# Kernel tuning notes

Hardware: AMD Instinct MI355X
Metric: run time of the kernel (lower is better)

The kernel has to match this reference:

```python
import jax, jax.numpy as jnp
import numpy as np

EM_DIM = 64
GROUP = 16
DIM_IN = 1024


def _position_embedding(boxes, part_boxes):
    # boxes: [N,4], part_boxes: [P,4] -> [N,P,EM_DIM]
    xmin, ymin, xmax, ymax = [boxes[:, i:i + 1] for i in range(4)]            # [N,1]
    pxmin, pymin, pxmax, pymax = [part_boxes[:, i:i + 1].T for i in range(4)]  # [1,P]
    bw = xmax - xmin + 1.0
    bh = ymax - ymin + 1.0
    pw = pxmax - pxmin + 1.0
    ph = pymax - pymin + 1.0
    cx = 0.5 * (xmin + xmax)
    cy = 0.5 * (ymin + ymax)
    pcx = 0.5 * (pxmin + pxmax)
    pcy = 0.5 * (pymin + pymax)
    dx = jnp.abs((cx - pcx) / bw)
    dy = jnp.abs((cy - pcy) / bh)
    dx = jnp.log(jnp.where(dx < 1e-3, 1e-3, dx))
    dy = jnp.log(jnp.where(dy < 1e-3, 1e-3, dy))
    dw = jnp.log(pw / bw)
    dh = jnp.log(ph / bh)
    pos = jnp.stack([dx, dy, dw, dh], axis=2)                                  # [N,P,4]
    em_range = jnp.arange(EM_DIM // 8, dtype=pos.dtype) / (EM_DIM // 8)        # [8]
    em_mat = jnp.power(jnp.asarray(1000.0, pos.dtype), em_range)               # [8]
    div = (100.0 * pos)[..., None] / em_mat                                    # [N,P,4,8]
    emb = jnp.concatenate([jnp.sin(div), jnp.cos(div)], axis=3)                # [N,P,4,16]
    return emb.reshape(pos.shape[0], pos.shape[1], EM_DIM)


def _single_relation(boxes, part_boxes, bf, pf, Wg_w, Wg_b, Wq_w, Wq_b, Wk_w, Wk_b, conv_w, conv_b):
    N = bf.shape[0]
    P = pf.shape[0]
    emb = _position_embedding(boxes, part_boxes)                               # [N,P,64]
    pos_feat = jax.nn.relu(emb @ Wg_w.T + Wg_b)                                # [N,P,G]
    att_weight = jnp.transpose(pos_feat, (0, 2, 1))                            # [N,G,P]
    q = (bf @ Wq_w.T + Wq_b).reshape(N, GROUP, EM_DIM)                         # [N,G,64]
    k = (pf @ Wk_w.T + Wk_b).reshape(P, GROUP, EM_DIM)                         # [P,G,64]
    att = jnp.einsum('ngd,pgd->ngp', q, k) * (1.0 / GROUP)                     # [N,G,P]
    att_weight = jnp.where(att_weight < 1e-6, 1e-6, att_weight)
    sm = jax.nn.softmax(jnp.log(att_weight) + att, axis=2)                     # [N,G,P]
    out = jnp.einsum('ngp,pc->ngc', sm, pf)                                    # [N,G,dim_in]
    # grouped 1x1 conv: group g maps dim_in channels -> EM_DIM channels
    w3 = conv_w.reshape(GROUP, EM_DIM, DIM_IN)
    rel = jnp.einsum('ngc,goc->ngo', out, w3).reshape(N, GROUP * EM_DIM) + conv_b
    return rel                                                                  # [N, G*EM_DIM]


def setup_inputs() -> dict:
    key = jax.random.key(0)
    ks = jax.random.split(key, 12)
    N_TOT, P_TOT = 2048, 2048

    def make_rois(k1, k2, n, n1):
        xy = jax.random.uniform(k1, (n, 2), jnp.float32) * 800.0
        wh = jax.random.uniform(k2, (n, 2), jnp.float32) * 200.0 + 16.0
        boxes = jnp.concatenate([xy, xy + wh], axis=1)
        idx = jnp.concatenate([jnp.zeros((n1, 1)), jnp.ones((n - n1, 1))], axis=0).astype(jnp.float32)
        return jnp.concatenate([idx, boxes], axis=1)

    rois = make_rois(ks[0], ks[1], N_TOT, 1024)
    part_rois = make_rois(ks[2], ks[3], P_TOT, 1024)
    box_feats = jax.random.normal(ks[4], (N_TOT, DIM_IN), jnp.float32)
    part_feats = jax.random.normal(ks[5], (P_TOT, DIM_IN), jnp.float32)
    xav_g = float(np.sqrt(6.0 / (EM_DIM + GROUP)))
    xav_qk = float(np.sqrt(6.0 / (DIM_IN + GROUP * EM_DIM)))
    Wg_w = jax.random.uniform(ks[6], (GROUP, EM_DIM), jnp.float32, -xav_g, xav_g)
    Wg_b = jnp.zeros((GROUP,), jnp.float32)
    Wq_w = jax.random.uniform(ks[7], (GROUP * EM_DIM, DIM_IN), jnp.float32, -xav_qk, xav_qk)
    Wq_b = jnp.zeros((GROUP * EM_DIM,), jnp.float32)
    Wk_w = jax.random.uniform(ks[8], (GROUP * EM_DIM, DIM_IN), jnp.float32, -xav_qk, xav_qk)
    Wk_b = jnp.zeros((GROUP * EM_DIM,), jnp.float32)
    conv_w = jax.random.normal(ks[9], (GROUP * EM_DIM, DIM_IN), jnp.float32) * 0.02
    conv_b = jnp.zeros((GROUP * EM_DIM,), jnp.float32)
    return {"rois": rois, "part_rois": part_rois, "box_feats": box_feats,
            "part_feats": part_feats, "Wg_w": Wg_w, "Wg_b": Wg_b,
            "Wq_w": Wq_w, "Wq_b": Wq_b, "Wk_w": Wk_w, "Wk_b": Wk_b,
            "conv_w": conv_w, "conv_b": conv_b, "n1_boxes": 1024, "n1_parts": 1024}


def reference(rois, part_rois, box_feats, part_feats, Wg_w, Wg_b, Wq_w, Wq_b,
              Wk_w, Wk_b, conv_w, conv_b, n1_boxes, n1_parts):
    boxes = rois[:, 1:5]
    part_boxes = part_rois[:, 1:5]
    params = (Wg_w, Wg_b, Wq_w, Wq_b, Wk_w, Wk_b, conv_w, conv_b)
    rel1 = _single_relation(boxes[:n1_boxes], part_boxes[:n1_parts],
                            box_feats[:n1_boxes], part_feats[:n1_parts], *params)
    rel2 = _single_relation(boxes[n1_boxes:], part_boxes[n1_parts:],
                            box_feats[n1_boxes:], part_feats[n1_parts:], *params)
    return jnp.concatenate([rel1, rel2], axis=0)  # [N_total, GROUP*EM_DIM]
```

## Files before the change

### kernel.cpp

```cpp
#include <hip/hip_runtime.h>

typedef unsigned short u16;
using short8  = __attribute__((ext_vector_type(8))) short;
using float4v = __attribute__((ext_vector_type(4))) float;

__device__ __forceinline__ u16 f2bf(float f) {
    union { float f; unsigned u; } v; v.f = f;
    unsigned r = (v.u + 0x7fff + ((v.u >> 16) & 1)) >> 16;
    return (u16)r;
}
__device__ __forceinline__ float bf2f(u16 h) {
    union { unsigned u; float f; } v; v.u = ((unsigned)h) << 16; return v.f;
}
__device__ __forceinline__ unsigned pkbf(float lo, float hi) {
    unsigned d;
    asm("v_cvt_pk_bf16_f32 %0, %1, %2" : "=v"(d) : "v"(lo), "v"(hi));
    return d;
}
__device__ __forceinline__ float sin_rev(float r) {
    float f, s;
    asm("v_fract_f32 %0, %1" : "=v"(f) : "v"(r));
    asm("v_sin_f32 %0, %1" : "=v"(s) : "v"(f));
    return s;
}
__device__ __forceinline__ void dma16(const void* g, void* l) {
    __builtin_amdgcn_global_load_lds((const __attribute__((address_space(1))) void*)g,
                                     (__attribute__((address_space(3))) void*)l, 16, 0, 0);
}

__device__ __forceinline__ void cvt4(const float* __restrict__ s, u16* __restrict__ o, int i) {
    float4 v = ((const float4*)s)[i];
    uint2 r; r.x = pkbf(v.x, v.y); r.y = pkbf(v.z, v.w);
    ((uint2*)o)[i] = r;
}

__global__ __launch_bounds__(256)
void cvt_all(const float* __restrict__ s0, const float* __restrict__ s1,
             const float* __restrict__ s2, const float* __restrict__ s3,
             const float* __restrict__ s4, const float* __restrict__ prois,
             u16* __restrict__ o0, u16* __restrict__ o1, u16* __restrict__ o2,
             u16* __restrict__ o3, u16* __restrict__ o4, float4* __restrict__ PD,
             int na4, int nb4, int nw4, int PT) {
    int i = blockIdx.x * 256 + threadIdx.x;
    if (i < na4) { cvt4(s0, o0, i); return; }
    i -= na4;
    if (i < nb4) { cvt4(s1, o1, i); return; }
    i -= nb4;
    if (i < nw4) { cvt4(s2, o2, i); return; }
    i -= nw4;
    if (i < nw4) { cvt4(s3, o3, i); return; }
    i -= nw4;
    if (i < nw4) { cvt4(s4, o4, i); return; }
    i -= nw4;
    if (i < PT) {
        const float* pr = prois + (size_t)i * 5;
        float pxmin = pr[1], pymin = pr[2], pxmax = pr[3], pymax = pr[4];
        PD[i] = make_float4(0.5f * (pxmin + pxmax), 0.5f * (pymin + pymax),
                            __logf(pxmax - pxmin + 1.0f), __logf(pymax - pymin + 1.0f));
    }
}

__global__ __launch_bounds__(256)
void proj_posw(const u16* __restrict__ Ab, const u16* __restrict__ Pb,
               const u16* __restrict__ Wqb, const u16* __restrict__ Wkb,
               const u16* __restrict__ Cwb, const float* __restrict__ bq,
               const float* __restrict__ bk, u16* __restrict__ Qb,
               u16* __restrict__ Kb, u16* __restrict__ PVt,
               const float* __restrict__ rois, const float4* __restrict__ PD,
               const float* __restrict__ Wg_w, const float* __restrict__ Wg_b,
               u16* __restrict__ POSW, const int* __restrict__ n1b_p,
               const int* __restrict__ n1p_p, int PT) {
    __shared__ __align__(16) u16 SH[16896];

    const int grp = blockIdx.x / 11, rem = blockIdx.x % 11;
    const int t = threadIdx.x;
    const int w = t >> 6, lane = t & 63;
    const int fm = lane & 15, quad = lane >> 4;

    if (rem < 3) {
        u16* As = SH;
        u16* Ws = SH + 8192;
        u16* Tr = SH;
        const int pb = grp * 3 + rem;
        const int z = pb >> 8;
        const int m0 = ((pb >> 4) & 15) * 128, j0 = (pb & 15) * 64;
        const u16* A = (z == 0) ? Ab : Pb;
        const u16* W = (z == 0) ? Wqb : (z == 1 ? Wkb : Cwb);
        const int wm = w >> 1, wn = w & 1;
        const int lr = lane >> 3, lc = lane & 7, gch = lc ^ lr;

        float4v zero4 = {0.f, 0.f, 0.f, 0.f};
        float4v acc[4][2];
#pragma unroll
        for (int i = 0; i < 4; ++i) { acc[i][0] = zero4; acc[i][1] = zero4; }

        for (int k0 = 0; k0 < 1024; k0 += 64) {
#pragma unroll
            for (int i = 0; i < 4; ++i) {
                int row = w * 32 + i * 8 + lr;
                dma16(A + (size_t)(m0 + row) * 1024 + k0 + gch * 8,
                      As + (w * 32 + i * 8) * 64 + lane * 8);
            }
#pragma unroll
            for (int i = 0; i < 2; ++i) {
                int row = w * 16 + i * 8 + lr;
                dma16(W + (size_t)(j0 + row) * 1024 + k0 + gch * 8,
                      Ws + (w * 16 + i * 8) * 64 + lane * 8);
            }
            __syncthreads();
#pragma unroll
            for (int ks = 0; ks < 2; ++ks) {
                int c = ks * 4 + quad;
                short8 af[4], bf[2];
#pragma unroll
                for (int i = 0; i < 4; ++i) {
                    int ra = wm * 64 + i * 16 + fm;
                    af[i] = *(const short8*)(As + ra * 64 + ((c ^ (ra & 7)) * 8));
                }
#pragma unroll
                for (int j = 0; j < 2; ++j) {
                    int rb = wn * 32 + j * 16 + fm;
                    bf[j] = *(const short8*)(Ws + rb * 64 + ((c ^ (rb & 7)) * 8));
                }
#pragma unroll
                for (int i = 0; i < 4; ++i)
#pragma unroll
                    for (int j = 0; j < 2; ++j)
                        acc[i][j] = __builtin_amdgcn_mfma_f32_16x16x32_bf16(af[i], bf[j], acc[i][j], 0, 0, 0);
            }
            __syncthreads();
        }

        if (z < 2) {
            u16* O = z ? Kb : Qb;
            const float* bias = z ? bk : bq;
#pragma unroll
            for (int j = 0; j < 2; ++j) {
                int jl = wn * 32 + j * 16 + fm;
                float bb = bias[j0 + jl];
#pragma unroll
                for (int i = 0; i < 4; ++i) {
                    int mlb = wm * 64 + i * 16 + quad * 4;
#pragma unroll
                    for (int r = 0; r < 4; ++r)
                        Tr[(mlb + r) * 68 + jl] = f2bf(acc[i][j][r] + bb);
                }
            }
            __syncthreads();
#pragma unroll
            for (int i2 = 0; i2 < 4; ++i2) {
                int f = i2 * 2048 + t * 8;
                int ml = f >> 6, jl = f & 63;
                union { uint2 u2[2]; short8 s8; } uu;
                uu.u2[0] = *(const uint2*)(Tr + ml * 68 + jl);
                uu.u2[1] = *(const uint2*)(Tr + ml * 68 + jl + 4);
                *(short8*)(O + (size_t)(m0 + ml) * 1024 + j0 + jl) = uu.s8;
            }
        } else {
#pragma unroll
            for (int j = 0; j < 2; ++j) {
                int jl = wn * 32 + j * 16 + fm;
#pragma unroll
                for (int i = 0; i < 4; ++i) {
                    int mlb = wm * 64 + i * 16 + quad * 4;
                    uint2 pk;
                    pk.x = pkbf(acc[i][j][0], acc[i][j][1]);
                    pk.y = pkbf(acc[i][j][2], acc[i][j][3]);
                    *(uint2*)(Tr + jl * 136 + mlb) = pk;
                }
            }
            __syncthreads();
#pragma unroll
            for (int i2 = 0; i2 < 4; ++i2) {
                int f = i2 * 2048 + t * 8;
                int jl = f >> 7, ml = f & 127;
                union { uint2 u2[2]; short8 s8; } uu;
                uu.u2[0] = *(const uint2*)(Tr + jl * 136 + ml);
                uu.u2[1] = *(const uint2*)(Tr + jl * 136 + ml + 4);
                *(short8*)(PVt + (size_t)(j0 + jl) * PT + m0 + ml) = uu.s8;
            }
        }
        return;
    }

    u16* Wl = SH + w * 4224;

    const int n = grp * 8 + (rem - 3);
    const int n1b = *n1b_p, n1p = *n1p_p;
    const int hh = (n >= n1b) ? 1 : 0;
    const int p0 = hh ? n1p : 0;
    const int Ph = hh ? (PT - n1p) : n1p;

    float xmin = rois[n * 5 + 1], ymin = rois[n * 5 + 2];
    float xmax = rois[n * 5 + 3], ymax = rois[n * 5 + 4];
    float bw = xmax - xmin + 1.0f, bh = ymax - ymin + 1.0f;
    float cx = 0.5f * (xmin + xmax), cy = 0.5f * (ymin + ymax);

    const int jA = quad >> 1, trig = quad & 1;
    float cA   = (jA == 0) ? cx : cy;
    float invA = (jA == 0) ? (1.0f / bw) : (1.0f / bh);
    float lB   = (jA == 0) ? __logf(bw) : __logf(bh);
    float toff = trig ? 0.25f : 0.0f;

    const int g_ = fm;
    short8 b1, b2;
    {
        const float* w1 = Wg_w + g_ * 64 + quad * 8;
        const float* w2 = Wg_w + g_ * 64 + 32 + quad * 8;
        unsigned* p1 = (unsigned*)&b1;
        unsigned* p2 = (unsigned*)&b2;
#pragma unroll
        for (int kk = 0; kk < 4; ++kk) {
            p1[kk] = pkbf(w1[2 * kk], w1[2 * kk + 1]);
            p2[kk] = pkbf(w2[2 * kk], w2[2 * kk + 1]);
        }
    }
    float wgb = Wg_b[g_];

    const float inv_em[8] = {1.0f, 0.4216965034f, 0.1778279410f, 0.0749894209f,
                             0.0316227766f, 0.0133352143f, 0.0056234133f, 0.0023713737f};
    const float REV = 15.91549431f;
    const int prange = Ph >> 2;
    const int pb0 = w * prange;

    float4 pd_c = PD[p0 + pb0 + fm];

#pragma unroll 2
    for (int pt = 0; pt < 16; ++pt) {
        float4 pd_n;
        if (pt < 15) pd_n = PD[p0 + pb0 + pt * 16 + 16 + fm];
        float pc = (jA == 0) ? pd_c.x : pd_c.y;
        float lp = (jA == 0) ? pd_c.z : pd_c.w;
        float posA = __logf(fmaxf(fabsf(cA - pc) * invA, 0.001f));
        float posB = lp - lB;
        float br1 = posA * REV, br2 = posB * REV;
        float e1[8], e2[8];
#pragma unroll
        for (int k = 0; k < 8; ++k) {
            e1[k] = sin_rev(fmaf(br1, inv_em[k], toff));
            e2[k] = sin_rev(fmaf(br2, inv_em[k], toff));
        }
        short8 a1, a2;
        unsigned* pa1 = (unsigned*)&a1;
        unsigned* pa2 = (unsigned*)&a2;
#pragma unroll
        for (int kk = 0; kk < 4; ++kk) {
            pa1[kk] = pkbf(e1[2 * kk], e1[2 * kk + 1]);
            pa2[kk] = pkbf(e2[2 * kk], e2[2 * kk + 1]);
        }
        float4v acc = {wgb, wgb, wgb, wgb};
        acc = __builtin_amdgcn_mfma_f32_16x16x32_bf16(a1, b1, acc, 0, 0, 0);
        acc = __builtin_amdgcn_mfma_f32_16x16x32_bf16(a2, b2, acc, 0, 0, 0);

        float w0  = fmaxf(acc[0], 1e-6f);
        float w1v = fmaxf(acc[1], 1e-6f);
        float w2v = fmaxf(acc[2], 1e-6f);
        float w3v = fmaxf(acc[3], 1e-6f);
        uint2 wp; wp.x = pkbf(w0, w1v); wp.y = pkbf(w2v, w3v);
        *(uint2*)(Wl + pt * 264 + lane * 4) = wp;

        pd_c = pd_n;
    }

    const int p8 = (lane & 31) * 8;
    const int halfg = lane >> 5;
    const int itq = p8 >> 4;
    const int q0 = (p8 >> 2) & 3;
#pragma unroll
    for (int s = 0; s < 8; ++s) {
        int gg = s * 2 + halfg;
        union { uint2 u2[2]; short8 s8; } uu;
        uu.u2[0] = *(const uint2*)(Wl + itq * 264 + (q0 * 16 + gg) * 4);
        uu.u2[1] = *(const uint2*)(Wl + itq * 264 + ((q0 + 1) * 16 + gg) * 4);
        *(short8*)(POSW + ((size_t)n * 16 + gg) * 1024 + pb0 + p8) = uu.s8;
    }
}

__global__ __launch_bounds__(256)
void fused_rel(const u16* __restrict__ Qb, const u16* __restrict__ Kb,
               const u16* __restrict__ POSW, const u16* __restrict__ PVt,
               const float* __restrict__ conv_b, float* __restrict__ OUT,
               const int* __restrict__ n1b_p, const int* __restrict__ n1p_p, int PT) {
    __shared__ __align__(16) u16 Qs[64 * 64];
    __shared__ __align__(16) u16 Ks[2][64 * 64];
    __shared__ __align__(16) u16 Ps[2][64 * 64];
    __shared__ __align__(16) u16 Vs[2][64 * 64];
    __shared__ __align__(16) u16 Wt[4][16 * 64];

    const int n0 = blockIdx.x * 64, g = blockIdx.y;
    const int n1b = *n1b_p, n1p = *n1p_p;
    const int hh = (n0 >= n1b) ? 1 : 0;
    const int p0 = hh ? n1p : 0;
    const int Ph = hh ? (PT - n1p) : n1p;
    const int t = threadIdx.x;
    const int w = t >> 6, lane = t & 63;
    const int lr = lane >> 3, lc = lane & 7, gch = lc ^ lr;
    const int fm = lane & 15, quad = lane >> 4;
    const int swz = fm & 7;

    const int row0 = w * 16 + lr, row1 = w * 16 + 8 + lr;
    const size_t kb0 = (size_t)(p0 + row0) * 1024 + g * 64 + gch * 8;
    const size_t kb1 = (size_t)(p0 + row1) * 1024 + g * 64 + gch * 8;
    const size_t vb0 = (size_t)(g * 64 + row0) * PT + p0 + gch * 8;
    const size_t vb1 = (size_t)(g * 64 + row1) * PT + p0 + gch * 8;
    const size_t pbs0 = ((size_t)(n0 + row0) * 16 + g) * 1024 + gch * 8;
    const size_t pbs1 = ((size_t)(n0 + row1) * 16 + g) * 1024 + gch * 8;
    const int d0 = (w * 16) * 64 + lane * 8;
    const int d1 = (w * 16 + 8) * 64 + lane * 8;

    dma16(Qb + (size_t)(n0 + row0) * 1024 + g * 64 + gch * 8, Qs + d0);
    dma16(Qb + (size_t)(n0 + row1) * 1024 + g * 64 + gch * 8, Qs + d1);
    {
        uint4 ka = *(const uint4*)(Kb + kb0), kbv = *(const uint4*)(Kb + kb1);
        uint4 va = *(const uint4*)(PVt + vb0), vb = *(const uint4*)(PVt + vb1);
        uint4 pa = *(const uint4*)(POSW + pbs0), pbv = *(const uint4*)(POSW + pbs1);
        *(uint4*)(Ks[0] + d0) = ka;  *(uint4*)(Ks[0] + d1) = kbv;
        *(uint4*)(Vs[0] + d0) = va;  *(uint4*)(Vs[0] + d1) = vb;
        *(uint4*)(Ps[0] + d0) = pa;  *(uint4*)(Ps[0] + d1) = pbv;
    }
    uint4 prH0 = *(const uint4*)(POSW + pbs0 + 64);
    uint4 prH1 = *(const uint4*)(POSW + pbs1 + 64);

    float4v zero4 = {0.f, 0.f, 0.f, 0.f};
    float4v oacc[4];
#pragma unroll
    for (int ob = 0; ob < 4; ++ob) oacc[ob] = zero4;
    float rsum = 0.0f;

    __syncthreads();

    const int nloc = w * 16 + fm;
    short8 qf[2];
#pragma unroll
    for (int kd = 0; kd < 2; ++kd) {
        int c = kd * 4 + quad;
        qf[kd] = *(const short8*)(Qs + nloc * 64 + ((c ^ swz) * 8));
    }
    u16* wrow = Wt[w] + fm * 64;

    const int NPT = Ph >> 6;
    for (int pt = 0; pt < NPT; ++pt) {
        const int cur = pt & 1, nxt = cur ^ 1;
        const u16* ks_ = Ks[cur];
        const u16* ps_ = Ps[cur];
        const u16* vs_ = Vs[cur];
        const bool have1 = (pt + 1 < NPT), have2 = (pt + 2 < NPT);

        uint4 kra, krb, vra, vrb, prN0, prN1;
        if (have1) {
            size_t o = (size_t)(pt + 1) * 65536;
            kra = *(const uint4*)(Kb + kb0 + o);
            krb = *(const uint4*)(Kb + kb1 + o);
            vra = *(const uint4*)(PVt + vb0 + (pt + 1) * 64);
            vrb = *(const uint4*)(PVt + vb1 + (pt + 1) * 64);
        }
        if (have2) {
            prN0 = *(const uint4*)(POSW + pbs0 + (pt + 2) * 64);
            prN1 = *(const uint4*)(POSW + pbs1 + (pt + 2) * 64);
        }

        float4v atc[4];
#pragma unroll
        for (int pi = 0; pi < 4; ++pi) atc[pi] = zero4;
#pragma unroll
        for (int kd = 0; kd < 2; ++kd) {
            int c = kd * 4 + quad;
#pragma unroll
            for (int pi = 0; pi < 4; ++pi) {
                int rp = pi * 16 + fm;
                short8 kf = *(const short8*)(ks_ + rp * 64 + ((c ^ swz) * 8));
                atc[pi] = __builtin_amdgcn_mfma_f32_16x16x32_bf16(kf, qf[kd], atc[pi], 0, 0, 0);
            }
        }

#pragma unroll
        for (int pi = 0; pi < 4; ++pi) {
            int co = ((pi * 2 + (quad >> 1)) ^ swz) * 8 + (quad & 1) * 4;
            uint2 pwp = *(const uint2*)(ps_ + nloc * 64 + co);
            const u16* pww = (const u16*)&pwp;
            float wv0 = bf2f(pww[0]) * __expf(atc[pi][0] * 0.0625f);
            float wv1 = bf2f(pww[1]) * __expf(atc[pi][1] * 0.0625f);
            float wv2 = bf2f(pww[2]) * __expf(atc[pi][2] * 0.0625f);
            float wv3 = bf2f(pww[3]) * __expf(atc[pi][3] * 0.0625f);
            rsum += (wv0 + wv1) + (wv2 + wv3);
            uint2 wp; wp.x = pkbf(wv0, wv1); wp.y = pkbf(wv2, wv3);
            *(uint2*)(wrow + co) = wp;
        }

#pragma unroll
        for (int m = 0; m < 2; ++m) {
            short8 af = *(const short8*)(wrow + (((m * 4 + quad) ^ swz) * 8));
#pragma unroll
            for (int ob = 0; ob < 4; ++ob) {
                int ro = ob * 16 + fm;
                short8 vf = *(const short8*)(vs_ + ro * 64 + (((m * 4 + quad) ^ swz) * 8));
                oacc[ob] = __builtin_amdgcn_mfma_f32_16x16x32_bf16(af, vf, oacc[ob], 0, 0, 0);
            }
        }

        if (have1) {
            *(uint4*)(Ks[nxt] + d0) = kra;  *(uint4*)(Ks[nxt] + d1) = krb;
            *(uint4*)(Vs[nxt] + d0) = vra;  *(uint4*)(Vs[nxt] + d1) = vrb;
            *(uint4*)(Ps[nxt] + d0) = prH0; *(uint4*)(Ps[nxt] + d1) = prH1;
            prH0 = prN0; prH1 = prN1;
        }

        __syncthreads();
    }

    float s = rsum;
    s += __shfl_xor(s, 16, 64);
    s += __shfl_xor(s, 32, 64);
    float inv[4];
#pragma unroll
    for (int r = 0; r < 4; ++r)
        inv[r] = 1.0f / __shfl(s, quad * 4 + r, 64);

    float bb[4];
#pragma unroll
    for (int ob = 0; ob < 4; ++ob) bb[ob] = conv_b[g * 64 + ob * 16 + fm];
#pragma unroll
    for (int ob = 0; ob < 4; ++ob)
#pragma unroll
        for (int r = 0; r < 4; ++r) {
            int nn = n0 + w * 16 + quad * 4 + r;
            OUT[(size_t)nn * 1024 + g * 64 + ob * 16 + fm] = oacc[ob][r] * inv[r] + bb[ob];
        }
}

extern "C" void kernel_launch(void* const* d_in, const int* in_sizes, int n_in,
                              void* d_out, int out_size, void* d_ws, size_t ws_size,
                              hipStream_t stream) {
    const float* rois   = (const float*)d_in[0];
    const float* prois  = (const float*)d_in[1];
    const float* bfeat  = (const float*)d_in[2];
    const float* pfeat  = (const float*)d_in[3];
    const float* Wg_w   = (const float*)d_in[4];
    const float* Wg_b   = (const float*)d_in[5];
    const float* Wq_w   = (const float*)d_in[6];
    const float* Wq_b   = (const float*)d_in[7];
    const float* Wk_w   = (const float*)d_in[8];
    const float* Wk_b   = (const float*)d_in[9];
    const float* conv_w = (const float*)d_in[10];
    const float* conv_b = (const float*)d_in[11];
    const int*   n1b    = (const int*)d_in[12];
    const int*   n1p    = (const int*)d_in[13];

    const int NT = in_sizes[2] / 1024;
    const int PT = in_sizes[3] / 1024;

    u16* Qb   = (u16*)d_ws;
    u16* Kb   = Qb + (size_t)NT * 1024;
    u16* PVt  = Kb + (size_t)PT * 1024;
    float4* PD = (float4*)(PVt + (size_t)1024 * PT);
    u16* POSW = (u16*)(PD + PT);
    u16* Ab   = POSW + (size_t)NT * 16 * 1024;
    u16* Pb   = Ab + (size_t)NT * 1024;
    u16* Wqb  = Pb + (size_t)PT * 1024;
    u16* Wkb  = Wqb + 1024 * 1024;
    u16* Cwb  = Wkb + 1024 * 1024;

    dim3 blk(256);
    int nf4 = NT * 1024 / 4, pf4 = PT * 1024 / 4, wf4 = 1024 * 1024 / 4;
    int tot = nf4 + pf4 + 3 * wf4 + PT;
    cvt_all<<<dim3((tot + 255) / 256), blk, 0, stream>>>(
        bfeat, pfeat, Wq_w, Wk_w, conv_w, prois, Ab, Pb, Wqb, Wkb, Cwb, PD,
        nf4, pf4, wf4, PT);

    proj_posw<<<dim3(256 * 11), blk, 0, stream>>>(Ab, Pb, Wqb, Wkb, Cwb,
                                                  Wq_b, Wk_b, Qb, Kb, PVt,
                                                  rois, PD, Wg_w, Wg_b, POSW,
                                                  n1b, n1p, PT);
    fused_rel<<<dim3(NT / 64, 16), blk, 0, stream>>>(Qb, Kb, POSW, PVt, conv_b,
                                                     (float*)d_out, n1b, n1p, PT);
}
```

Before: 168.8 us.

## Shrink LDS footprint in projection and fused relation kernels

proj_posw now builds the position-weight tile in two halves of 128 parts each. That halves the per-wave staging buffer and cuts the block's shared memory from about 33KB to 24KB. In fused_rel, Q fragments are loaded straight from global memory into registers instead of going through a shared-memory tile, and the position-weight tile becomes single-buffered. Single buffering is safe because each wave only reads and writes its own rows. The aim is to raise occupancy and remove one LDS round trip. The cost is an extra write/read phase in proj_posw and uncoalesced per-lane Q loads.

```diff
diff --git a/kernel.cpp b/kernel.cpp
--- a/kernel.cpp
+++ b/kernel.cpp
@@ -70,7 +70,7 @@
                const float* __restrict__ Wg_w, const float* __restrict__ Wg_b,
                u16* __restrict__ POSW, const int* __restrict__ n1b_p,
                const int* __restrict__ n1p_p, int PT) {
-    __shared__ __align__(16) u16 SH[16896];
+    __shared__ __align__(16) u16 SH[12288];
 
     const int grp = blockIdx.x / 11, rem = blockIdx.x % 11;
     const int t = threadIdx.x;
@@ -183,7 +183,7 @@
         return;
     }
 
-    u16* Wl = SH + w * 4224;
+    u16* Wl = SH + w * 2112;
 
     const int n = grp * 8 + (rem - 3);
     const int n1b = *n1b_p, n1p = *n1p_p;
@@ -225,54 +225,57 @@
 
     float4 pd_c = PD[p0 + pb0 + fm];
 
+    for (int half = 0; half < 2; ++half) {
 #pragma unroll 2
-    for (int pt = 0; pt < 16; ++pt) {
-        float4 pd_n;
-        if (pt < 15) pd_n = PD[p0 + pb0 + pt * 16 + 16 + fm];
-        float pc = (jA == 0) ? pd_c.x : pd_c.y;
-        float lp = (jA == 0) ? pd_c.z : pd_c.w;
-        float posA = __logf(fmaxf(fabsf(cA - pc) * invA, 0.001f));
-        float posB = lp - lB;
-        float br1 = posA * REV, br2 = posB * REV;
-        float e1[8], e2[8];
-#pragma unroll
-        for (int k = 0; k < 8; ++k) {
-            e1[k] = sin_rev(fmaf(br1, inv_em[k], toff));
-            e2[k] = sin_rev(fmaf(br2, inv_em[k], toff));
-        }
-        short8 a1, a2;
-        unsigned* pa1 = (unsigned*)&a1;
-        unsigned* pa2 = (unsigned*)&a2;
-#pragma unroll
-        for (int kk = 0; kk < 4; ++kk) {
-            pa1[kk] = pkbf(e1[2 * kk], e1[2 * kk + 1]);
-            pa2[kk] = pkbf(e2[2 * kk], e2[2 * kk + 1]);
-        }
-        float4v acc = {wgb, wgb, wgb, wgb};
-        acc = __builtin_amdgcn_mfma_f32_16x16x32_bf16(a1, b1, acc, 0, 0, 0);
-        acc = __builtin_amdgcn_mfma_f32_16x16x32_bf16(a2, b2, acc, 0, 0, 0);
-
-        float w0  = fmaxf(acc[0], 1e-6f);
-        float w1v = fmaxf(acc[1], 1e-6f);
-        float w2v = fmaxf(acc[2], 1e-6f);
-        float w3v = fmaxf(acc[3], 1e-6f);
-        uint2 wp; wp.x = pkbf(w0, w1v); wp.y = pkbf(w2v, w3v);
-        *(uint2*)(Wl + pt * 264 + lane * 4) = wp;
-
-        pd_c = pd_n;
-    }
-
-    const int p8 = (lane & 31) * 8;
-    const int halfg = lane >> 5;
-    const int itq = p8 >> 4;
-    const int q0 = (p8 >> 2) & 3;
-#pragma unroll
-    for (int s = 0; s < 8; ++s) {
-        int gg = s * 2 + halfg;
-        union { uint2 u2[2]; short8 s8; } uu;
-        uu.u2[0] = *(const uint2*)(Wl + itq * 264 + (q0 * 16 + gg) * 4);
-        uu.u2[1] = *(const uint2*)(Wl + itq * 264 + ((q0 + 1) * 16 + gg) * 4);
-        *(short8*)(POSW + ((size_t)n * 16 + gg) * 1024 + pb0 + p8) = uu.s8;
+        for (int pt8 = 0; pt8 < 8; ++pt8) {
+            int pt = half * 8 + pt8;
+            float4 pd_n;
+            if (pt < 15) pd_n = PD[p0 + pb0 + pt * 16 + 16 + fm];
+            float pc = (jA == 0) ? pd_c.x : pd_c.y;
+            float lp = (jA == 0) ? pd_c.z : pd_c.w;
+            float posA = __logf(fmaxf(fabsf(cA - pc) * invA, 0.001f));
+            float posB = lp - lB;
+            float br1 = posA * REV, br2 = posB * REV;
+            float e1[8], e2[8];
+#pragma unroll
+            for (int k = 0; k < 8; ++k) {
+                e1[k] = sin_rev(fmaf(br1, inv_em[k], toff));
+                e2[k] = sin_rev(fmaf(br2, inv_em[k], toff));
+            }
+            short8 a1, a2;
+            unsigned* pa1 = (unsigned*)&a1;
+            unsigned* pa2 = (unsigned*)&a2;
+#pragma unroll
+            for (int kk = 0; kk < 4; ++kk) {
+                pa1[kk] = pkbf(e1[2 * kk], e1[2 * kk + 1]);
+                pa2[kk] = pkbf(e2[2 * kk], e2[2 * kk + 1]);
+            }
+            float4v acc = {wgb, wgb, wgb, wgb};
+            acc = __builtin_amdgcn_mfma_f32_16x16x32_bf16(a1, b1, acc, 0, 0, 0);
+            acc = __builtin_amdgcn_mfma_f32_16x16x32_bf16(a2, b2, acc, 0, 0, 0);
+
+            float w0  = fmaxf(acc[0], 1e-6f);
+            float w1v = fmaxf(acc[1], 1e-6f);
+            float w2v = fmaxf(acc[2], 1e-6f);
+            float w3v = fmaxf(acc[3], 1e-6f);
+            uint2 wp; wp.x = pkbf(w0, w1v); wp.y = pkbf(w2v, w3v);
+            *(uint2*)(Wl + pt8 * 264 + lane * 4) = wp;
+
+            pd_c = pd_n;
+        }
+        {
+            const int p8 = (lane & 15) * 8;
+            const int itq = p8 >> 4, q0 = (p8 >> 2) & 3;
+            const int phh = half * 128;
+#pragma unroll
+            for (int s = 0; s < 4; ++s) {
+                int gg = s * 4 + (lane >> 4);
+                union { uint2 u2[2]; short8 s8; } uu;
+                uu.u2[0] = *(const uint2*)(Wl + itq * 264 + (q0 * 16 + gg) * 4);
+                uu.u2[1] = *(const uint2*)(Wl + itq * 264 + ((q0 + 1) * 16 + gg) * 4);
+                *(short8*)(POSW + ((size_t)n * 16 + gg) * 1024 + pb0 + phh + p8) = uu.s8;
+            }
+        }
     }
 }
 
@@ -281,9 +284,8 @@
                const u16* __restrict__ POSW, const u16* __restrict__ PVt,
                const float* __restrict__ conv_b, float* __restrict__ OUT,
                const int* __restrict__ n1b_p, const int* __restrict__ n1p_p, int PT) {
-    __shared__ __align__(16) u16 Qs[64 * 64];
     __shared__ __align__(16) u16 Ks[2][64 * 64];
-    __shared__ __align__(16) u16 Ps[2][64 * 64];
+    __shared__ __align__(16) u16 Ps[64 * 64];
     __shared__ __align__(16) u16 Vs[2][64 * 64];
     __shared__ __align__(16) u16 Wt[4][16 * 64];
 
@@ -297,6 +299,7 @@
     const int lr = lane >> 3, lc = lane & 7, gch = lc ^ lr;
     const int fm = lane & 15, quad = lane >> 4;
     const int swz = fm & 7;
+    const int nloc = w * 16 + fm;
 
     const int row0 = w * 16 + lr, row1 = w * 16 + 8 + lr;
     const size_t kb0 = (size_t)(p0 + row0) * 1024 + g * 64 + gch * 8;
@@ -308,18 +311,20 @@
     const int d0 = (w * 16) * 64 + lane * 8;
     const int d1 = (w * 16 + 8) * 64 + lane * 8;
 
-    dma16(Qb + (size_t)(n0 + row0) * 1024 + g * 64 + gch * 8, Qs + d0);
-    dma16(Qb + (size_t)(n0 + row1) * 1024 + g * 64 + gch * 8, Qs + d1);
     {
         uint4 ka = *(const uint4*)(Kb + kb0), kbv = *(const uint4*)(Kb + kb1);
         uint4 va = *(const uint4*)(PVt + vb0), vb = *(const uint4*)(PVt + vb1);
         uint4 pa = *(const uint4*)(POSW + pbs0), pbv = *(const uint4*)(POSW + pbs1);
         *(uint4*)(Ks[0] + d0) = ka;  *(uint4*)(Ks[0] + d1) = kbv;
         *(uint4*)(Vs[0] + d0) = va;  *(uint4*)(Vs[0] + d1) = vb;
-        *(uint4*)(Ps[0] + d0) = pa;  *(uint4*)(Ps[0] + d1) = pbv;
+        *(uint4*)(Ps + d0) = pa;     *(uint4*)(Ps + d1) = pbv;
     }
     uint4 prH0 = *(const uint4*)(POSW + pbs0 + 64);
     uint4 prH1 = *(const uint4*)(POSW + pbs1 + 64);
+    short8 qf[2];
+#pragma unroll
+    for (int kd = 0; kd < 2; ++kd)
+        qf[kd] = *(const short8*)(Qb + (size_t)(n0 + nloc) * 1024 + g * 64 + (kd * 4 + quad) * 8);
 
     float4v zero4 = {0.f, 0.f, 0.f, 0.f};
     float4v oacc[4];
@@ -329,20 +334,12 @@
 
     __syncthreads();
 
-    const int nloc = w * 16 + fm;
-    short8 qf[2];
-#pragma unroll
-    for (int kd = 0; kd < 2; ++kd) {
-        int c = kd * 4 + quad;
-        qf[kd] = *(const short8*)(Qs + nloc * 64 + ((c ^ swz) * 8));
-    }
     u16* wrow = Wt[w] + fm * 64;
 
     const int NPT = Ph >> 6;
     for (int pt = 0; pt < NPT; ++pt) {
         const int cur = pt & 1, nxt = cur ^ 1;
         const u16* ks_ = Ks[cur];
-        const u16* ps_ = Ps[cur];
         const u16* vs_ = Vs[cur];
         const bool have1 = (pt + 1 < NPT), have2 = (pt + 2 < NPT);
 
@@ -376,7 +373,7 @@
 #pragma unroll
         for (int pi = 0; pi < 4; ++pi) {
             int co = ((pi * 2 + (quad >> 1)) ^ swz) * 8 + (quad & 1) * 4;
-            uint2 pwp = *(const uint2*)(ps_ + nloc * 64 + co);
+            uint2 pwp = *(const uint2*)(Ps + nloc * 64 + co);
             const u16* pww = (const u16*)&pwp;
             float wv0 = bf2f(pww[0]) * __expf(atc[pi][0] * 0.0625f);
             float wv1 = bf2f(pww[1]) * __expf(atc[pi][1] * 0.0625f);
@@ -401,7 +398,7 @@
         if (have1) {
             *(uint4*)(Ks[nxt] + d0) = kra;  *(uint4*)(Ks[nxt] + d1) = krb;
             *(uint4*)(Vs[nxt] + d0) = vra;  *(uint4*)(Vs[nxt] + d1) = vrb;
-            *(uint4*)(Ps[nxt] + d0) = prH0; *(uint4*)(Ps[nxt] + d1) = prH1;
+            *(uint4*)(Ps + d0) = prH0;      *(uint4*)(Ps + d1) = prH1;
             prH0 = prN0; prH1 = prN1;
         }
 
```

Result: slower. 173.0 us (+2.5%).

## Double-buffer projection GEMM tiles with register prefetch instead of direct LDS DMA

Applied to the files above, without the earlier changes.

Replaces the per-iteration global-to-LDS DMA followed by a barrier with a double-buffered scheme. The next K tile is loaded into registers while MFMAs run on the current LDS buffer, then stored to the other buffer, leaving one barrier per iteration. This is meant to hide global load latency behind compute. In exchange LDS use grows to 48KB and register pressure rises, which may lower occupancy.

```diff
diff --git a/kernel.cpp b/kernel.cpp
--- a/kernel.cpp
+++ b/kernel.cpp
@@ -70,7 +70,7 @@
                const float* __restrict__ Wg_w, const float* __restrict__ Wg_b,
                u16* __restrict__ POSW, const int* __restrict__ n1b_p,
                const int* __restrict__ n1p_p, int PT) {
-    __shared__ __align__(16) u16 SH[16896];
+    __shared__ __align__(16) u16 SH[24576];
 
     const int grp = blockIdx.x / 11, rem = blockIdx.x % 11;
     const int t = threadIdx.x;
@@ -78,8 +78,6 @@
     const int fm = lane & 15, quad = lane >> 4;
 
     if (rem < 3) {
-        u16* As = SH;
-        u16* Ws = SH + 8192;
         u16* Tr = SH;
         const int pb = grp * 3 + rem;
         const int z = pb >> 8;
@@ -89,25 +87,52 @@
         const int wm = w >> 1, wn = w & 1;
         const int lr = lane >> 3, lc = lane & 7, gch = lc ^ lr;
 
+        size_t ga[4], gw[2];
+        int da[4], dw[2];
+#pragma unroll
+        for (int i = 0; i < 4; ++i) {
+            ga[i] = (size_t)(m0 + w * 32 + i * 8 + lr) * 1024 + gch * 8;
+            da[i] = (w * 32 + i * 8) * 64 + lane * 8;
+        }
+#pragma unroll
+        for (int i = 0; i < 2; ++i) {
+            gw[i] = (size_t)(j0 + w * 16 + i * 8 + lr) * 1024 + gch * 8;
+            dw[i] = 16384 + (w * 16 + i * 8) * 64 + lane * 8;
+        }
+
         float4v zero4 = {0.f, 0.f, 0.f, 0.f};
         float4v acc[4][2];
 #pragma unroll
         for (int i = 0; i < 4; ++i) { acc[i][0] = zero4; acc[i][1] = zero4; }
 
-        for (int k0 = 0; k0 < 1024; k0 += 64) {
-#pragma unroll
-            for (int i = 0; i < 4; ++i) {
-                int row = w * 32 + i * 8 + lr;
-                dma16(A + (size_t)(m0 + row) * 1024 + k0 + gch * 8,
-                      As + (w * 32 + i * 8) * 64 + lane * 8);
-            }
-#pragma unroll
-            for (int i = 0; i < 2; ++i) {
-                int row = w * 16 + i * 8 + lr;
-                dma16(W + (size_t)(j0 + row) * 1024 + k0 + gch * 8,
-                      Ws + (w * 16 + i * 8) * 64 + lane * 8);
-            }
-            __syncthreads();
+        {
+            uint4 ar[4], wr[2];
+#pragma unroll
+            for (int i = 0; i < 4; ++i) ar[i] = *(const uint4*)(A + ga[i]);
+#pragma unroll
+            for (int i = 0; i < 2; ++i) wr[i] = *(const uint4*)(W + gw[i]);
+#pragma unroll
+            for (int i = 0; i < 4; ++i) *(uint4*)(SH + da[i]) = ar[i];
+#pragma unroll
+            for (int i = 0; i < 2; ++i) *(uint4*)(SH + dw[i]) = wr[i];
+        }
+        __syncthreads();
+
+        for (int kt = 0; kt < 16; ++kt) {
+            const int cur = kt & 1, nxt = cur ^ 1;
+            const int aCur = cur * 8192, wCur = cur * 4096;
+            const int aNxt = nxt * 8192, wNxt = nxt * 4096;
+            const bool more = kt < 15;
+            uint4 ar[4], wr[2];
+            if (more) {
+                const size_t k1 = (size_t)(kt + 1) * 64;
+#pragma unroll
+                for (int i = 0; i < 4; ++i) ar[i] = *(const uint4*)(A + ga[i] + k1);
+#pragma unroll
+                for (int i = 0; i < 2; ++i) wr[i] = *(const uint4*)(W + gw[i] + k1);
+            }
+            const u16* As = SH + aCur;
+            const u16* Ws = SH + 16384 + wCur;
 #pragma unroll
             for (int ks = 0; ks < 2; ++ks) {
                 int c = ks * 4 + quad;
@@ -127,6 +152,12 @@
 #pragma unroll
                     for (int j = 0; j < 2; ++j)
                         acc[i][j] = __builtin_amdgcn_mfma_f32_16x16x32_bf16(af[i], bf[j], acc[i][j], 0, 0, 0);
+            }
+            if (more) {
+#pragma unroll
+                for (int i = 0; i < 4; ++i) *(uint4*)(SH + aNxt + da[i]) = ar[i];
+#pragma unroll
+                for (int i = 0; i < 2; ++i) *(uint4*)(SH + wNxt + dw[i]) = wr[i];
             }
             __syncthreads();
         }
```

Result: no change. 171.5 us (+1.6%).

## Use angle-addition identity to precompute part-box trig terms for size embedding

Applied to the files above, without the earlier changes.

The log-size component of the position embedding, log(pw) - log(bw), is split with the sin/cos angle-addition identity. The sin and cos of the part-box term are precomputed once per part box in the conversion kernel and stored in a new workspace table. The box term is computed once per thread, so the inner loop replaces eight transcendental sin evaluations per iteration with FMAs. In exchange it adds global loads of 16 floats per iteration from the table and extra register pressure for the prefetched values, and it may change numerics slightly.

```diff
diff --git a/kernel.cpp b/kernel.cpp
--- a/kernel.cpp
+++ b/kernel.cpp
@@ -27,6 +27,8 @@
     __builtin_amdgcn_global_load_lds((const __attribute__((address_space(1))) void*)g,
                                      (__attribute__((address_space(3))) void*)l, 16, 0, 0);
 }
+
+#define REVC 15.91549431f
 
 __device__ __forceinline__ void cvt4(const float* __restrict__ s, u16* __restrict__ o, int i) {
     float4 v = ((const float4*)s)[i];
@@ -40,7 +42,7 @@
              const float* __restrict__ s4, const float* __restrict__ prois,
              u16* __restrict__ o0, u16* __restrict__ o1, u16* __restrict__ o2,
              u16* __restrict__ o3, u16* __restrict__ o4, float4* __restrict__ PD,
-             int na4, int nb4, int nw4, int PT) {
+             float* __restrict__ PTRIG, int na4, int nb4, int nw4, int PT) {
     int i = blockIdx.x * 256 + threadIdx.x;
     if (i < na4) { cvt4(s0, o0, i); return; }
     i -= na4;
@@ -53,10 +55,21 @@
     if (i < nw4) { cvt4(s4, o4, i); return; }
     i -= nw4;
     if (i < PT) {
+        const float inv_em[8] = {1.0f, 0.4216965034f, 0.1778279410f, 0.0749894209f,
+                                 0.0316227766f, 0.0133352143f, 0.0056234133f, 0.0023713737f};
         const float* pr = prois + (size_t)i * 5;
         float pxmin = pr[1], pymin = pr[2], pxmax = pr[3], pymax = pr[4];
-        PD[i] = make_float4(0.5f * (pxmin + pxmax), 0.5f * (pymin + pymax),
-                            __logf(pxmax - pxmin + 1.0f), __logf(pymax - pymin + 1.0f));
+        float lpw = __logf(pxmax - pxmin + 1.0f), lph = __logf(pymax - pymin + 1.0f);
+        PD[i] = make_float4(0.5f * (pxmin + pxmax), 0.5f * (pymin + pymax), lpw, lph);
+        float aw = lpw * REVC, ah = lph * REVC;
+#pragma unroll
+        for (int k = 0; k < 8; ++k) {
+            float a = aw * inv_em[k], b = ah * inv_em[k];
+            PTRIG[(size_t)k * PT + i]        = sin_rev(a);
+            PTRIG[(size_t)(8 + k) * PT + i]  = sin_rev(a + 0.25f);
+            PTRIG[(size_t)(16 + k) * PT + i] = sin_rev(b);
+            PTRIG[(size_t)(24 + k) * PT + i] = sin_rev(b + 0.25f);
+        }
     }
 }
 
@@ -67,6 +80,7 @@
                const float* __restrict__ bk, u16* __restrict__ Qb,
                u16* __restrict__ Kb, u16* __restrict__ PVt,
                const float* __restrict__ rois, const float4* __restrict__ PD,
+               const float* __restrict__ PTRIG,
                const float* __restrict__ Wg_w, const float* __restrict__ Wg_b,
                u16* __restrict__ POSW, const int* __restrict__ n1b_p,
                const int* __restrict__ n1p_p, int PT) {
@@ -202,6 +216,23 @@
     float lB   = (jA == 0) ? __logf(bw) : __logf(bh);
     float toff = trig ? 0.25f : 0.0f;
 
+    const float inv_em[8] = {1.0f, 0.4216965034f, 0.1778279410f, 0.0749894209f,
+                             0.0316227766f, 0.0133352143f, 0.0056234133f, 0.0023713737f};
+
+    float cb[8], sbx[8];
+    {
+        float sgn = trig ? 1.0f : -1.0f;
+        float bn = lB * REVC;
+#pragma unroll
+        for (int k = 0; k < 8; ++k) {
+            float b = bn * inv_em[k];
+            cb[k]  = sin_rev(b + 0.25f);
+            sbx[k] = sgn * sin_rev(b);
+        }
+    }
+    const float* TU = PTRIG + (size_t)(jA * 16 + trig * 8) * PT;
+    const float* TV = PTRIG + (size_t)(jA * 16 + (1 - trig) * 8) * PT;
+
     const int g_ = fm;
     short8 b1, b2;
     {
@@ -217,29 +248,44 @@
     }
     float wgb = Wg_b[g_];
 
-    const float inv_em[8] = {1.0f, 0.4216965034f, 0.1778279410f, 0.0749894209f,
-                             0.0316227766f, 0.0133352143f, 0.0056234133f, 0.0023713737f};
-    const float REV = 15.91549431f;
     const int prange = Ph >> 2;
     const int pb0 = w * prange;
 
-    float4 pd_c = PD[p0 + pb0 + fm];
+    int ppc = p0 + pb0 + fm;
+    float4 pd_c = PD[ppc];
+    float Uc[8], Vc[8];
+#pragma unroll
+    for (int k = 0; k < 8; ++k) {
+        Uc[k] = TU[k * PT + ppc];
+        Vc[k] = TV[k * PT + ppc];
+    }
 
 #pragma unroll 2
     for (int pt = 0; pt < 16; ++pt) {
         float4 pd_n;
-        if (pt < 15) pd_n = PD[p0 + pb0 + pt * 16 + 16 + fm];
+        float Un[8], Vn[8];
+        if (pt < 15) {
+            pd_n = PD[ppc + 16];
+#pragma unroll
+            for (int k = 0; k < 8; ++k) {
+                Un[k] = TU[k * PT + ppc + 16];
+                Vn[k] = TV[k * PT + ppc + 16];
+            }
+        }
+
         float pc = (jA == 0) ? pd_c.x : pd_c.y;
-        float lp = (jA == 0) ? pd_c.z : pd_c.w;
         float posA = __logf(fmaxf(fabsf(cA - pc) * invA, 0.001f));
-        float posB = lp - lB;
-        float br1 = posA * REV, br2 = posB * REV;
-        float e1[8], e2[8];
-#pragma unroll
-        for (int k = 0; k < 8; ++k) {
+        float br1 = posA * REVC;
+        float e1[8];
+#pragma unroll
+        for (int k = 0; k < 8; ++k)
             e1[k] = sin_rev(fmaf(br1, inv_em[k], toff));
-            e2[k] = sin_rev(fmaf(br2, inv_em[k], toff));
-        }
+
+        float e2[8];
+#pragma unroll
+        for (int k = 0; k < 8; ++k)
+            e2[k] = fmaf(Uc[k], cb[k], Vc[k] * sbx[k]);
+
         short8 a1, a2;
         unsigned* pa1 = (unsigned*)&a1;
         unsigned* pa2 = (unsigned*)&a2;
@@ -260,6 +306,9 @@
         *(uint2*)(Wl + pt * 264 + lane * 4) = wp;
 
         pd_c = pd_n;
+#pragma unroll
+        for (int k = 0; k < 8; ++k) { Uc[k] = Un[k]; Vc[k] = Vn[k]; }
+        ppc += 16;
     }
 
     const int p8 = (lane & 31) * 8;
@@ -453,7 +502,8 @@
     u16* Kb   = Qb + (size_t)NT * 1024;
     u16* PVt  = Kb + (size_t)PT * 1024;
     float4* PD = (float4*)(PVt + (size_t)1024 * PT);
-    u16* POSW = (u16*)(PD + PT);
+    float* PTRIG = (float*)(PD + PT);
+    u16* POSW = (u16*)(PTRIG + (size_t)32 * PT);
     u16* Ab   = POSW + (size_t)NT * 16 * 1024;
     u16* Pb   = Ab + (size_t)NT * 1024;
     u16* Wqb  = Pb + (size_t)PT * 1024;
@@ -465,11 +515,11 @@
     int tot = nf4 + pf4 + 3 * wf4 + PT;
     cvt_all<<<dim3((tot + 255) / 256), blk, 0, stream>>>(
         bfeat, pfeat, Wq_w, Wk_w, conv_w, prois, Ab, Pb, Wqb, Wkb, Cwb, PD,
-        nf4, pf4, wf4, PT);
+        PTRIG, nf4, pf4, wf4, PT);
 
     proj_posw<<<dim3(256 * 11), blk, 0, stream>>>(Ab, Pb, Wqb, Wkb, Cwb,
                                                   Wq_b, Wk_b, Qb, Kb, PVt,
-                                                  rois, PD, Wg_w, Wg_b, POSW,
+                                                  rois, PD, PTRIG, Wg_w, Wg_b, POSW,
                                                   n1b, n1p, PT);
     fused_rel<<<dim3(NT / 64, 16), blk, 0, stream>>>(Qb, Kb, POSW, PVt, conv_b,
                                                      (float*)d_out, n1b, n1p, PT);
```

Result: slower. 183.8 us (+8.9%).
